# Optimization experiments

Measured on AMD Instinct MI355X. Metric: run time of the kernel, lower is better.

The kernel has to match this reference:

```python
import jax, jax.numpy as jnp
import numpy as np

B, S, D, H, DFF = 2, 2048, 1024, 16, 4096
DH = D // H
EPS = 1e-12


def _layer_norm(x, g, b):
    mu = jnp.mean(x, axis=-1, keepdims=True)
    var = jnp.mean(jnp.square(x - mu), axis=-1, keepdims=True)
    return (x - mu) * jax.lax.rsqrt(var + EPS) * g + b


def setup_inputs() -> dict:
    key = jax.random.key(0)
    ks = jax.random.split(key, 12)
    s = 0.02
    return {
        "query": jax.random.normal(ks[0], (B, S, D), jnp.float32),
        "key_in": jax.random.normal(ks[1], (B, S, D), jnp.float32),
        "value_in": jax.random.normal(ks[2], (B, S, D), jnp.float32),
        "attention_mask": jnp.zeros((B, 1, 1, S), jnp.float32),
        # weights stored [in, out] (i.e., torch Linear weight transposed)
        "Wq": jax.random.normal(ks[3], (D, D), jnp.float32) * s,
        "bq": jnp.zeros((D,), jnp.float32),
        "Wk": jax.random.normal(ks[4], (D, D), jnp.float32) * s,
        "bk": jnp.zeros((D,), jnp.float32),
        "Wv": jax.random.normal(ks[5], (D, D), jnp.float32) * s,
        "bv": jnp.zeros((D,), jnp.float32),
        "Wo": jax.random.normal(ks[6], (D, D), jnp.float32) * s,
        "bo": jnp.zeros((D,), jnp.float32),
        "ln1_g": jnp.ones((D,), jnp.float32),
        "ln1_b": jnp.zeros((D,), jnp.float32),
        "Wi": jax.random.normal(ks[7], (D, DFF), jnp.float32) * s,
        "bi": jnp.zeros((DFF,), jnp.float32),
        "Wd": jax.random.normal(ks[8], (DFF, D), jnp.float32) * s,
        "bd": jnp.zeros((D,), jnp.float32),
        "ln2_g": jnp.ones((D,), jnp.float32),
        "ln2_b": jnp.zeros((D,), jnp.float32),
    }


def reference(query, key_in, value_in, attention_mask, Wq, bq, Wk, bk, Wv, bv,
              Wo, bo, ln1_g, ln1_b, Wi, bi, Wd, bd, ln2_g, ln2_b):
    # projections -> [B, H, S, DH]
    q = (query @ Wq + bq).reshape(B, S, H, DH).transpose(0, 2, 1, 3)
    k = (key_in @ Wk + bk).reshape(B, S, H, DH).transpose(0, 2, 1, 3)
    v = (value_in @ Wv + bv).reshape(B, S, H, DH).transpose(0, 2, 1, 3)
    # eager attention: full [B,H,S,S] score matrix, as in the source
    scores = jnp.einsum("bhqd,bhkd->bhqk", q, k) / jnp.sqrt(jnp.float32(DH))
    scores = scores + attention_mask
    probs = jax.nn.softmax(scores, axis=-1)  # dropout p=0 -> identity
    ctx = jnp.einsum("bhqk,bhkd->bhqd", probs, v)
    ctx = ctx.transpose(0, 2, 1, 3).reshape(B, S, D)
    attn_out = ctx @ Wo + bo
    attn_out = _layer_norm(attn_out + query, ln1_g, ln1_b)
    inter = jax.nn.gelu(attn_out @ Wi + bi, approximate=False)
    layer_out = inter @ Wd + bd
    return _layer_norm(layer_out + attn_out, ln2_g, ln2_b)
```

## Files before the change

kernel.cpp:

```cpp
#include <hip/hip_runtime.h>
#include <hip/hip_bf16.h>
#include <cmath>

#define B_   2
#define S_   2048
#define D_   1024
#define H_   16
#define DFF_ 4096
#define DH_  64
#define M_   (B_*S_)

typedef __bf16 bfx8 __attribute__((ext_vector_type(8)));
typedef __bf16 bfx4 __attribute__((ext_vector_type(4)));
typedef float  fx4  __attribute__((ext_vector_type(4)));

__device__ __forceinline__ float fast_exp2(float x) {
  float r;
  asm volatile("v_exp_f32 %0, %1" : "=v"(r) : "v"(x));
  return r;
}

__device__ __forceinline__ float fast_erf(float x) {
  float ax = fabsf(x);
  float t  = __builtin_amdgcn_rcpf(fmaf(0.3275911f, ax, 1.0f));
  float p  = fmaf(1.061405429f, t, -1.453152027f);
  p = fmaf(p, t, 1.421413741f);
  p = fmaf(p, t, -0.284496736f);
  p = fmaf(p, t, 0.254829592f);
  p = p * t;
  float e  = fast_exp2(-ax * ax * 1.44269504f);
  float r  = 1.0f - p * e;
  return copysignf(r, x);
}

__device__ __forceinline__ void gload_lds16(const void* g, void* l) {
  __builtin_amdgcn_global_load_lds((__attribute__((address_space(1))) void*)(g),
                                   (__attribute__((address_space(3))) void*)(l),
                                   16, 0, 0);
}

struct PrepArgs {
  const float* win[6]; __bf16* wout[6];
  const float* cin[3]; __bf16* cout[3];
};

__global__ __launch_bounds__(256)
void prep_kernel(PrepArgs a) {
  int bid = blockIdx.x;
  if (bid < 12288) {
    __shared__ float t[32][33];
    int wsel, tr, tc, R, C;
    if (bid < 4096) {
      wsel = bid >> 10; int l = bid & 1023;
      tr = l >> 5; tc = l & 31; R = D_; C = D_;
    } else if (bid < 8192) {
      wsel = 4; int l = bid - 4096;
      tr = l >> 7; tc = l & 127; R = D_; C = DFF_;
    } else {
      wsel = 5; int l = bid - 8192;
      tr = l >> 5; tc = l & 31; R = DFF_; C = D_;
    }
    const float* in = a.win[wsel];
    __bf16* out = a.wout[wsel];
    int r0 = tr * 32, c0 = tc * 32;
    int tx = threadIdx.x & 31, ty = threadIdx.x >> 5;
#pragma unroll
    for (int j = 0; j < 4; ++j) {
      int r = ty + j * 8;
      t[r][tx] = in[(size_t)(r0 + r) * C + c0 + tx];
    }
    __syncthreads();
#pragma unroll
    for (int j = 0; j < 4; ++j) {
      int c = ty + j * 8;
      out[(size_t)(c0 + c) * R + r0 + tx] = (__bf16)t[tx][c];
    }
  } else {
    int l = bid - 12288;
    int z = l >> 12;
    int i = ((l & 4095) * 256 + threadIdx.x) * 4;
    float4 v = *(const float4*)(a.cin[z] + i);
    bfx4 o;
    o[0] = (__bf16)v.x; o[1] = (__bf16)v.y; o[2] = (__bf16)v.z; o[3] = (__bf16)v.w;
    *(bfx4*)(a.cout[z] + i) = o;
  }
}

template<int MODE, int TBN>
__global__ __launch_bounds__(256)
void gemm_kernel(const __bf16* __restrict__ A, const __bf16* __restrict__ Bt,
                 const float* __restrict__ bias, const void* __restrict__ res,
                 void* __restrict__ out, int Ndim, int Kdim) {
  __shared__ alignas(16) __bf16 As[2 * 128 * 64];
  __shared__ alignas(16) __bf16 Bs[2 * TBN * 64];
  const int tid  = threadIdx.x;
  const int lane = tid & 63;
  const int w    = tid >> 6;
  const int wm   = w >> 1, wn = w & 1;
  constexpr int NF = TBN / 32;

  const int gX  = gridDim.x;
  const int nwg = gridDim.x * gridDim.y;
  int lid = blockIdx.y * gX + blockIdx.x;
  int swz = (lid & 7) * (nwg >> 3) + (lid >> 3);
  const int m0 = (swz / gX) * 128, n0 = (swz % gX) * TBN;

  fx4 acc[4][NF];
#pragma unroll
  for (int i = 0; i < 4; ++i)
#pragma unroll
    for (int j = 0; j < NF; ++j) acc[i][j] = {0.f, 0.f, 0.f, 0.f};

  const int KT = Kdim / 64;

  auto stage = [&](int kt, int buf) {
    const int kb0 = kt * 64;
#pragma unroll
    for (int i = 0; i < 4; ++i) {
      int o   = tid * 16 + i * 4096;
      int row = o >> 7, cb = o & 127;
      int cbs = cb ^ ((row & 7) << 4);
      gload_lds16((const char*)A + ((size_t)(m0 + row) * Kdim + kb0) * 2 + cbs,
                  (char*)As + buf * 16384 + o);
    }
#pragma unroll
    for (int i = 0; i < NF; ++i) {
      int o   = tid * 16 + i * 4096;
      int row = o >> 7, cb = o & 127;
      int cbs = cb ^ ((row & 7) << 4);
      gload_lds16((const char*)Bt + ((size_t)(n0 + row) * Kdim + kb0) * 2 + cbs,
                  (char*)Bs + buf * (TBN * 128) + o);
    }
  };

  stage(0, 0);
  asm volatile("s_waitcnt vmcnt(0)" ::: "memory");
  __builtin_amdgcn_s_barrier();
  __builtin_amdgcn_sched_barrier(0);

  for (int kt = 0; kt < KT; ++kt) {
    if (kt + 1 < KT) stage(kt + 1, (kt + 1) & 1);
    __builtin_amdgcn_sched_barrier(0);
    if (kt > 0) {
      if (kt + 1 < KT) {
        if constexpr (TBN == 64) asm volatile("s_waitcnt vmcnt(6)" ::: "memory");
        else                     asm volatile("s_waitcnt vmcnt(8)" ::: "memory");
      } else {
        asm volatile("s_waitcnt vmcnt(0)" ::: "memory");
      }
      __builtin_amdgcn_s_barrier();
      __builtin_amdgcn_sched_barrier(0);
    }
    const char* Ab = (const char*)As + (kt & 1) * 16384;
    const char* Bb = (const char*)Bs + (kt & 1) * (TBN * 128);

#pragma unroll
    for (int kk = 0; kk < 2; ++kk) {
      bfx8 afr[4], bfr[NF];
      const int cb = kk * 64 + ((lane >> 4) << 4);
#pragma unroll
      for (int mf = 0; mf < 4; ++mf) {
        int row = wm * 64 + mf * 16 + (lane & 15);
        afr[mf] = *(const bfx8*)(Ab + row * 128 + (cb ^ ((row & 7) << 4)));
      }
#pragma unroll
      for (int nf = 0; nf < NF; ++nf) {
        int row = wn * (TBN / 2) + nf * 16 + (lane & 15);
        bfr[nf] = *(const bfx8*)(Bb + row * 128 + (cb ^ ((row & 7) << 4)));
      }
#pragma unroll
      for (int mf = 0; mf < 4; ++mf)
#pragma unroll
        for (int nf = 0; nf < NF; ++nf)
          acc[mf][nf] = __builtin_amdgcn_mfma_f32_16x16x32_bf16(afr[mf], bfr[nf],
                                                                acc[mf][nf], 0, 0, 0);
    }
    __builtin_amdgcn_s_barrier();
    __builtin_amdgcn_sched_barrier(0);
  }

#pragma unroll
  for (int mf = 0; mf < 4; ++mf) {
#pragma unroll
    for (int nf = 0; nf < NF; ++nf) {
      int col = n0 + wn * (TBN / 2) + nf * 16 + (lane & 15);
      float bvl = bias[col];
#pragma unroll
      for (int r = 0; r < 4; ++r) {
        int rowg = m0 + wm * 64 + mf * 16 + ((lane >> 4) << 2) + r;
        float v = acc[mf][nf][r] + bvl;
        if (MODE == 2) v = 0.5f * v * (1.0f + fast_erf(v * 0.70710678118654752f));
        if (MODE == 4) v += (float)((const __bf16*)res)[(size_t)rowg * Ndim + col];
        if (MODE == 1) ((float*)out)[(size_t)rowg * Ndim + col] = v;
        else           ((__bf16*)out)[(size_t)rowg * Ndim + col] = (__bf16)v;
      }
    }
  }
}

__device__ __forceinline__ void stage_a256(const __bf16* __restrict__ A, int m0,
                                           int Kdim, int tile, int h, char* Asm) {
  char* dst = Asm + (tile & 1) * 32768;
  const int kb0 = tile * 64;
  const int tid = threadIdx.x;
#pragma unroll
  for (int it = 0; it < 2; ++it) {
    int o = tid * 16 + it * 8192;
    int lrow = o >> 7, cb = o & 127;
    int r = (lrow & 63) + h * 64 + ((lrow >> 6) << 7);
    int csrc = cb ^ ((r & 7) << 4);
    gload_lds16((const char*)A + ((size_t)(m0 + r) * Kdim + kb0) * 2 + csrc,
                dst + r * 128 + cb);
  }
}
__device__ __forceinline__ void stage_b256(const __bf16* __restrict__ Bt, int n0,
                                           int Kdim, int tile, int h, char* Bsm) {
  char* dst = Bsm + (tile & 1) * 32768;
  const int kb0 = tile * 64;
  const int tid = threadIdx.x;
#pragma unroll
  for (int it = 0; it < 2; ++it) {
    int o = tid * 16 + it * 8192;
    int lrow = o >> 7, cb = o & 127;
    int r = h * 128 + lrow;
    int csrc = cb ^ ((r & 7) << 4);
    gload_lds16((const char*)Bt + ((size_t)(n0 + r) * Kdim + kb0) * 2 + csrc,
                dst + r * 128 + cb);
  }
}

template<int MODE>
__device__ __forceinline__ void gemm256_body(const __bf16* __restrict__ A,
                                             const __bf16* __restrict__ Bt,
                                             const float* __restrict__ bias,
                                             void* __restrict__ out,
                                             int Ndim, int Kdim, int m0, int n0) {
  extern __shared__ char smem[];
  char* Asm = smem;
  char* Bsm = smem + 65536;
  const int tid  = threadIdx.x;
  const int lane = tid & 63;
  const int w    = tid >> 6;
  const int wm   = w >> 2;
  const int wn   = w & 3;
  const int g    = lane >> 4;
  const int ql   = lane & 15;
  const int KT   = Kdim / 64;

  fx4 acc[8][4];
#pragma unroll
  for (int i = 0; i < 8; ++i)
#pragma unroll
    for (int j = 0; j < 4; ++j) acc[i][j] = {0.f, 0.f, 0.f, 0.f};

  stage_a256(A, m0, Kdim, 0, 0, Asm);
  stage_a256(A, m0, Kdim, 0, 1, Asm);
  stage_b256(Bt, n0, Kdim, 0, 0, Bsm);
  stage_b256(Bt, n0, Kdim, 0, 1, Bsm);
  stage_a256(A, m0, Kdim, 1, 0, Asm);
  asm volatile("s_waitcnt vmcnt(2)" ::: "memory");
  __builtin_amdgcn_s_barrier();
  __builtin_amdgcn_sched_barrier(0);

  for (int t = 0; t < KT; ++t) {
    const char* Ab = Asm + (t & 1) * 32768;
    const char* Bb = Bsm + (t & 1) * 32768;
#pragma unroll
    for (int p = 0; p < 4; ++p) {
      const int ah = p >> 1, kk = p & 1;
      if (p == 0 && t + 1 < KT) stage_a256(A, m0, Kdim, t + 1, 1, Asm);
      if (p == 1 && t + 1 < KT) stage_b256(Bt, n0, Kdim, t + 1, 0, Bsm);
      if (p == 2 && t + 1 < KT) stage_b256(Bt, n0, Kdim, t + 1, 1, Bsm);
      if (p == 3 && t + 2 < KT) stage_a256(A, m0, Kdim, t + 2, 0, Asm);
      __builtin_amdgcn_sched_barrier(0);

      bfx8 af[4], bf[4];
      const int cbv = kk * 64 + g * 16;
#pragma unroll
      for (int j = 0; j < 4; ++j) {
        int arow = wm * 128 + (ah * 4 + j) * 16 + ql;
        af[j] = *(const bfx8*)(Ab + arow * 128 + (cbv ^ ((arow & 7) << 4)));
      }
#pragma unroll
      for (int nf = 0; nf < 4; ++nf) {
        int brow = wn * 64 + nf * 16 + ql;
        bf[nf] = *(const bfx8*)(Bb + brow * 128 + (cbv ^ ((brow & 7) << 4)));
      }
      __builtin_amdgcn_sched_barrier(0);
      __builtin_amdgcn_s_barrier();
      asm volatile("s_waitcnt lgkmcnt(0)" ::: "memory");
      __builtin_amdgcn_sched_barrier(0);
      __builtin_amdgcn_s_setprio(1);
#pragma unroll
      for (int j = 0; j < 4; ++j)
#pragma unroll
        for (int nf = 0; nf < 4; ++nf)
          acc[ah * 4 + j][nf] = __builtin_amdgcn_mfma_f32_16x16x32_bf16(
              af[j], bf[nf], acc[ah * 4 + j][nf], 0, 0, 0);
      __builtin_amdgcn_s_setprio(0);
      __builtin_amdgcn_s_barrier();
      __builtin_amdgcn_sched_barrier(0);
    }
    if (t + 1 < KT) {
      if (t + 2 < KT) asm volatile("s_waitcnt vmcnt(2)" ::: "memory");
      else            asm volatile("s_waitcnt vmcnt(0)" ::: "memory");
      __builtin_amdgcn_s_barrier();
      __builtin_amdgcn_sched_barrier(0);
    }
  }

#pragma unroll
  for (int mf = 0; mf < 8; ++mf) {
#pragma unroll
    for (int nf = 0; nf < 4; ++nf) {
      int col = n0 + wn * 64 + nf * 16 + ql;
      float bvl = bias[col];
      if (MODE == 5) {
        int rowg0 = m0 + wm * 128 + mf * 16 + g * 4;
        int bb = rowg0 >> 11, s = rowg0 & 2047;
        int hh = col >> 6, dh = col & 63;
        bfx4 o;
#pragma unroll
        for (int r = 0; r < 4; ++r) o[r] = (__bf16)(acc[mf][nf][r] + bvl);
        *(bfx4*)((__bf16*)out + (((size_t)(bb * 16 + hh) * 64 + dh) * 2048 + s)) = o;
      } else {
#pragma unroll
        for (int r = 0; r < 4; ++r) {
          int rowg = m0 + wm * 128 + mf * 16 + g * 4 + r;
          float v = acc[mf][nf][r] + bvl;
          if (MODE == 2) v = 0.5f * v * (1.0f + fast_erf(v * 0.70710678118654752f));
          if (MODE == 1) ((float*)out)[(size_t)rowg * Ndim + col] = v;
          else          ((__bf16*)out)[(size_t)rowg * Ndim + col] = (__bf16)v;
        }
      }
    }
  }
}

template<int MODE>
__global__ __launch_bounds__(512)
void gemm256_kernel(const __bf16* __restrict__ A, const __bf16* __restrict__ Bt,
                    const float* __restrict__ bias, void* __restrict__ out,
                    int Ndim, int Kdim) {
  const int gX  = gridDim.x;
  const int nwg = gridDim.x * gridDim.y;
  int lid = blockIdx.y * gX + blockIdx.x;
  int swz = (lid & 7) * (nwg >> 3) + (lid >> 3);
  gemm256_body<MODE>(A, Bt, bias, out, Ndim, Kdim,
                     (swz / gX) * 256, (swz % gX) * 256);
}

struct QKVArgs {
  const __bf16* A[3]; const __bf16* Bt[3]; const float* bias[3]; __bf16* out[3];
};

__global__ __launch_bounds__(512)
void qkv256_kernel(QKVArgs args, int Ndim, int Kdim) {
  int z = blockIdx.z;
  const int gX  = gridDim.x;
  const int nwg = gridDim.x * gridDim.y;
  int lid = blockIdx.y * gX + blockIdx.x;
  int swz = (lid & 7) * (nwg >> 3) + (lid >> 3);
  int m0 = (swz / gX) * 256, n0 = (swz % gX) * 256;
  if (z == 2)
    gemm256_body<5>(args.A[2], args.Bt[2], args.bias[2], (void*)args.out[2],
                    Ndim, Kdim, m0, n0);
  else
    gemm256_body<0>(args.A[z], args.Bt[z], args.bias[z], (void*)args.out[z],
                    Ndim, Kdim, m0, n0);
}

__global__ __launch_bounds__(512)
void attn_kernel(const __bf16* __restrict__ Qb, const __bf16* __restrict__ Kb,
                 const __bf16* __restrict__ Vt, const float* __restrict__ mask,
                 __bf16* __restrict__ ctx) {
  __shared__ alignas(16) __bf16 Ks[3 * 64 * 64];
  __shared__ alignas(16) __bf16 Vs[3 * 64 * 64];
  __shared__ alignas(16) __bf16 Ps[8 * 16 * 64];
  __shared__ alignas(16) float  Ms[2048];

  const int tid  = threadIdx.x;
  const int lane = tid & 63;
  const int w    = tid >> 6;
  const int g    = lane >> 4;
  const int ql   = lane & 15;
  const int bh   = blockIdx.y;
  const int b    = bh >> 4;
  const int h    = bh & 15;
  const int q0   = blockIdx.x * 128;

  const size_t kbase  = ((size_t)(b * S_)) * D_ + h * DH_;
  const size_t vtbase = (size_t)bh * DH_ * S_;
  const int NT = S_ / 64;

  char* Qsm = (char*)Ps;
  const size_t qbase = ((size_t)(b * S_) + q0) * D_ + h * DH_;
#pragma unroll
  for (int i = 0; i < 2; ++i) {
    int o   = tid * 16 + i * 8192;
    int row = o >> 7, cb = o & 127;
    int cbs = cb ^ ((row & 7) << 4);
    gload_lds16((const char*)Qb + (qbase + (size_t)row * D_) * 2 + cbs, Qsm + o);
  }
  {
    int o = tid * 16;
    gload_lds16((const char*)mask + (size_t)b * S_ * 4 + o, (char*)Ms + o);
  }
  {
    int o   = tid * 16;
    int row = o >> 7, cb = o & 127;
    int cbs = cb ^ ((row & 7) << 4);
    gload_lds16((const char*)Kb + (kbase + (size_t)row * D_) * 2 + cbs, (char*)Ks + o);
    gload_lds16((const char*)Vt + (vtbase + (size_t)row * S_) * 2 + cbs, (char*)Vs + o);
    gload_lds16((const char*)Kb + (kbase + (size_t)(64 + row) * D_) * 2 + cbs,
                (char*)Ks + 8192 + o);
    gload_lds16((const char*)Vt + (vtbase + (size_t)row * S_ + 64) * 2 + cbs,
                (char*)Vs + 8192 + o);
  }
  asm volatile("s_waitcnt vmcnt(4)" ::: "memory");
  __builtin_amdgcn_s_barrier();
  __builtin_amdgcn_sched_barrier(0);

  {
    float4 mv = *(float4*)((char*)Ms + tid * 16);
    mv.x *= 1.44269504f; mv.y *= 1.44269504f;
    mv.z *= 1.44269504f; mv.w *= 1.44269504f;
    *(float4*)((char*)Ms + tid * 16) = mv;
  }

  bfx8 aq[2];
  {
    int row = w * 16 + ql;
#pragma unroll
    for (int kk = 0; kk < 2; ++kk) {
      int cb = kk * 64 + g * 16;
      aq[kk] = *(const bfx8*)(Qsm + row * 128 + (cb ^ ((row & 7) << 4)));
    }
  }
  __syncthreads();
  asm volatile("s_waitcnt vmcnt(2)" ::: "memory");
  __builtin_amdgcn_s_barrier();
  __builtin_amdgcn_sched_barrier(0);

  fx4 acc[4];
  fx4 accl = {0.f, 0.f, 0.f, 0.f};
#pragma unroll
  for (int d = 0; d < 4; ++d) acc[d] = {0.f, 0.f, 0.f, 0.f};

  bfx8 ones;
#pragma unroll
  for (int j = 0; j < 8; ++j) ones[j] = (__bf16)1.0f;

  char* pw = (char*)Ps + w * 2048;
  const float SCL = 0.18033688f;

  for (int t = 0; t < NT; ++t) {
    const int kv0 = t * 64;
    if (t + 2 < NT) {
      int o   = tid * 16;
      int row = o >> 7, cb = o & 127;
      int cbs = cb ^ ((row & 7) << 4);
      int nkv = kv0 + 128;
      int bo  = ((t + 2) % 3) * 8192;
      gload_lds16((const char*)Kb + (kbase + (size_t)(nkv + row) * D_) * 2 + cbs,
                  (char*)Ks + bo + o);
      gload_lds16((const char*)Vt + (vtbase + (size_t)row * S_ + nkv) * 2 + cbs,
                  (char*)Vs + bo + o);
    }
    __builtin_amdgcn_sched_barrier(0);
    const char* Kc = (const char*)Ks + (t % 3) * 8192;
    const char* Vc = (const char*)Vs + (t % 3) * 8192;

    fx4 sc[4];
#pragma unroll
    for (int nf = 0; nf < 4; ++nf) sc[nf] = {0.f, 0.f, 0.f, 0.f};
#pragma unroll
    for (int kk = 0; kk < 2; ++kk) {
      const int cb = kk * 64 + g * 16;
      bfx8 bk[4];
#pragma unroll
      for (int nf = 0; nf < 4; ++nf) {
        int row = nf * 16 + ql;
        bk[nf] = *(const bfx8*)(Kc + row * 128 + (cb ^ ((row & 7) << 4)));
      }
      __builtin_amdgcn_s_setprio(1);
#pragma unroll
      for (int nf = 0; nf < 4; ++nf)
        sc[nf] = __builtin_amdgcn_mfma_f32_16x16x32_bf16(bk[nf], aq[kk], sc[nf], 0, 0, 0);
      __builtin_amdgcn_s_setprio(0);
    }

    float sv[4][4];
#pragma unroll
    for (int nf = 0; nf < 4; ++nf) {
      float4 mk = *(const float4*)((const char*)Ms + (kv0 + nf * 16 + g * 4) * 4);
      sv[nf][0] = fast_exp2(fmaf(sc[nf][0], SCL, mk.x));
      sv[nf][1] = fast_exp2(fmaf(sc[nf][1], SCL, mk.y));
      sv[nf][2] = fast_exp2(fmaf(sc[nf][2], SCL, mk.z));
      sv[nf][3] = fast_exp2(fmaf(sc[nf][3], SCL, mk.w));
    }

#pragma unroll
    for (int nf = 0; nf < 4; ++nf) {
      bfx4 pv;
      pv[0] = (__bf16)sv[nf][0]; pv[1] = (__bf16)sv[nf][1];
      pv[2] = (__bf16)sv[nf][2]; pv[3] = (__bf16)sv[nf][3];
      int c = (nf * 32 + g * 8) ^ ((ql & 7) << 4);
      *(bfx4*)(pw + ql * 128 + c) = pv;
    }

    asm volatile("s_waitcnt lgkmcnt(0)" ::: "memory");
    __builtin_amdgcn_sched_barrier(0);

#pragma unroll
    for (int kk = 0; kk < 2; ++kk) {
      int prow = ql;
      int cb   = kk * 64 + g * 16;
      bfx8 ap  = *(const bfx8*)((const char*)pw + prow * 128 + (cb ^ ((prow & 7) << 4)));
      __builtin_amdgcn_s_setprio(1);
#pragma unroll
      for (int d = 0; d < 4; ++d) {
        int vrow = d * 16 + ql;
        bfx8 bv  = *(const bfx8*)(Vc + vrow * 128 + (cb ^ ((vrow & 7) << 4)));
        acc[d] = __builtin_amdgcn_mfma_f32_16x16x32_bf16(ap, bv, acc[d], 0, 0, 0);
      }
      accl = __builtin_amdgcn_mfma_f32_16x16x32_bf16(ap, ones, accl, 0, 0, 0);
      __builtin_amdgcn_s_setprio(0);
    }

    if (t + 1 < NT) {
      if (t + 2 < NT) asm volatile("s_waitcnt vmcnt(2)" ::: "memory");
      else            asm volatile("s_waitcnt vmcnt(0)" ::: "memory");
      __builtin_amdgcn_s_barrier();
      __builtin_amdgcn_sched_barrier(0);
    }
  }

#pragma unroll
  for (int r = 0; r < 4; ++r) {
    float inv = 1.0f / accl[r];
    int qrow = q0 + w * 16 + g * 4 + r;
    size_t base = ((size_t)(b * S_) + qrow) * D_ + h * DH_;
#pragma unroll
    for (int d = 0; d < 4; ++d)
      ctx[base + d * 16 + ql] = (__bf16)(acc[d][r] * inv);
  }
}

template<bool WRITE_BF16>
__global__ __launch_bounds__(256)
void ln_kernel(const __bf16* __restrict__ a,
               const float* __restrict__ g, const float* __restrict__ beta,
               float* __restrict__ outf, __bf16* __restrict__ outb) {
  const int row = blockIdx.x;
  const int tid = threadIdx.x;
  const size_t base = (size_t)row * D_;
  bfx4 xa = *(const bfx4*)(a + base + tid * 4);
  float x[4] = {(float)xa[0], (float)xa[1], (float)xa[2], (float)xa[3]};
  float s = x[0] + x[1] + x[2] + x[3];
#pragma unroll
  for (int m = 1; m < 64; m <<= 1) s += __shfl_xor(s, m);
  __shared__ float red[8];
  if ((tid & 63) == 0) red[tid >> 6] = s;
  __syncthreads();
  float mu = (red[0] + red[1] + red[2] + red[3]) * (1.0f / D_);
  float v0 = 0.f;
#pragma unroll
  for (int i = 0; i < 4; ++i) { float d = x[i] - mu; v0 += d * d; }
#pragma unroll
  for (int m = 1; m < 64; m <<= 1) v0 += __shfl_xor(v0, m);
  if ((tid & 63) == 0) red[4 + (tid >> 6)] = v0;
  __syncthreads();
  float var = (red[4] + red[5] + red[6] + red[7]) * (1.0f / D_);
  float rs = rsqrtf(var + 1e-12f);
#pragma unroll
  for (int i = 0; i < 4; ++i) {
    int col = tid * 4 + i;
    x[i] = (x[i] - mu) * rs * g[col] + beta[col];
  }
  if (WRITE_BF16) {
    bfx4 o;
    o[0] = (__bf16)x[0]; o[1] = (__bf16)x[1]; o[2] = (__bf16)x[2]; o[3] = (__bf16)x[3];
    *(bfx4*)(outb + base + tid * 4) = o;
  } else {
    *(float4*)(outf + base + tid * 4) = make_float4(x[0], x[1], x[2], x[3]);
  }
}

extern "C" void kernel_launch(void* const* d_in, const int* in_sizes, int n_in,
                              void* d_out, int out_size, void* d_ws, size_t ws_size,
                              hipStream_t stream) {
  const float* query    = (const float*)d_in[0];
  const float* key_in   = (const float*)d_in[1];
  const float* value_in = (const float*)d_in[2];
  const float* mask     = (const float*)d_in[3];
  const float* Wq = (const float*)d_in[4];  const float* bq = (const float*)d_in[5];
  const float* Wk = (const float*)d_in[6];  const float* bk = (const float*)d_in[7];
  const float* Wv = (const float*)d_in[8];  const float* bv = (const float*)d_in[9];
  const float* Wo = (const float*)d_in[10]; const float* bo = (const float*)d_in[11];
  const float* ln1g = (const float*)d_in[12]; const float* ln1b = (const float*)d_in[13];
  const float* Wi = (const float*)d_in[14]; const float* bi = (const float*)d_in[15];
  const float* Wd = (const float*)d_in[16]; const float* bd = (const float*)d_in[17];
  const float* ln2g = (const float*)d_in[18]; const float* ln2b = (const float*)d_in[19];

  char* ws = (char*)d_ws;
  const size_t MB = 1ull << 20;
  if (ws_size < 112 * MB) return;

  __bf16* xq   = (__bf16*)(ws + 0 * MB);
  __bf16* xk   = (__bf16*)(ws + 8 * MB);
  __bf16* xv   = (__bf16*)(ws + 16 * MB);
  __bf16* x1b  = (__bf16*)(ws + 16 * MB);
  __bf16* qb   = (__bf16*)(ws + 24 * MB);
  __bf16* inter= (__bf16*)(ws + 24 * MB);
  __bf16* kb   = (__bf16*)(ws + 32 * MB);
  __bf16* alinb= (__bf16*)(ws + 40 * MB);
  __bf16* vt   = (__bf16*)(ws + 48 * MB);
  __bf16* ctxb = (__bf16*)(ws + 56 * MB);
  __bf16* ffb  = (__bf16*)(ws + 56 * MB);
  __bf16* wqt  = (__bf16*)(ws + 88 * MB);
  __bf16* wkt  = (__bf16*)(ws + 90 * MB);
  __bf16* wvt  = (__bf16*)(ws + 92 * MB);
  __bf16* wot  = (__bf16*)(ws + 94 * MB);
  __bf16* wit  = (__bf16*)(ws + 96 * MB);
  __bf16* wdt  = (__bf16*)(ws + 104 * MB);

  dim3 b256(256);

  PrepArgs pa;
  pa.win[0] = Wq; pa.win[1] = Wk; pa.win[2] = Wv; pa.win[3] = Wo;
  pa.win[4] = Wi; pa.win[5] = Wd;
  pa.wout[0] = wqt; pa.wout[1] = wkt; pa.wout[2] = wvt; pa.wout[3] = wot;
  pa.wout[4] = wit; pa.wout[5] = wdt;
  pa.cin[0] = query; pa.cin[1] = key_in; pa.cin[2] = value_in;
  pa.cout[0] = xq;   pa.cout[1] = xk;    pa.cout[2] = xv;
  prep_kernel<<<dim3(24576), b256, 0, stream>>>(pa);

  QKVArgs qa;
  qa.A[0] = xq;  qa.A[1] = xk;  qa.A[2] = xv;
  qa.Bt[0] = wqt; qa.Bt[1] = wkt; qa.Bt[2] = wvt;
  qa.bias[0] = bq; qa.bias[1] = bk; qa.bias[2] = bv;
  qa.out[0] = qb; qa.out[1] = kb; qa.out[2] = vt;
  qkv256_kernel<<<dim3(D_ / 256, M_ / 256, 3), dim3(512), 131072, stream>>>(qa, D_, D_);

  attn_kernel<<<dim3(S_ / 128, B_ * H_), dim3(512), 0, stream>>>(qb, kb, vt, mask, ctxb);

  gemm_kernel<4, 64><<<dim3(D_ / 64, M_ / 128), b256, 0, stream>>>(ctxb, wot, bo, xq, (void*)alinb, D_, D_);

  ln_kernel<true><<<dim3(M_), b256, 0, stream>>>(alinb, ln1g, ln1b, nullptr, x1b);

  gemm256_kernel<2><<<dim3(DFF_ / 256, M_ / 256), dim3(512), 131072, stream>>>(x1b, wit, bi, (void*)inter, DFF_, D_);

  gemm_kernel<4, 64><<<dim3(D_ / 64, M_ / 128), b256, 0, stream>>>(inter, wdt, bd, x1b, (void*)ffb, D_, DFF_);

  ln_kernel<false><<<dim3(M_), b256, 0, stream>>>(ffb, ln2g, ln2b, (float*)d_out, nullptr);
}
```

Measured before the change: 240.7 us.

## Prescale mask in prep kernel and double-buffer K/V in attention

Moves the log2(e) scaling of the attention mask into the prep kernel, writing a scaled copy to the workspace. The attention kernel now reads mask values straight from global memory each iteration instead of staging them in LDS. K/V staging drops from triple to double buffering with a full vmcnt(0) wait each step. This cuts LDS use (possibly raising occupancy) but shortens the prefetch distance and puts a global load in the inner loop.

```diff
diff --git a/kernel.cpp b/kernel.cpp
--- a/kernel.cpp
+++ b/kernel.cpp
@@ -42,6 +42,7 @@
 struct PrepArgs {
   const float* win[6]; __bf16* wout[6];
   const float* cin[3]; __bf16* cout[3];
+  const float* min;    float* mout;
 };
 
 __global__ __launch_bounds__(256)
@@ -75,7 +76,7 @@
       int c = ty + j * 8;
       out[(size_t)(c0 + c) * R + r0 + tx] = (__bf16)t[tx][c];
     }
-  } else {
+  } else if (bid < 24576) {
     int l = bid - 12288;
     int z = l >> 12;
     int i = ((l & 4095) * 256 + threadIdx.x) * 4;
@@ -83,6 +84,12 @@
     bfx4 o;
     o[0] = (__bf16)v.x; o[1] = (__bf16)v.y; o[2] = (__bf16)v.z; o[3] = (__bf16)v.w;
     *(bfx4*)(a.cout[z] + i) = o;
+  } else {
+    int i = ((bid - 24576) * 256 + threadIdx.x) * 4;
+    float4 v = *(const float4*)(a.min + i);
+    v.x *= 1.44269504f; v.y *= 1.44269504f;
+    v.z *= 1.44269504f; v.w *= 1.44269504f;
+    *(float4*)(a.mout + i) = v;
   }
 }
 
@@ -372,13 +379,11 @@
 
 __global__ __launch_bounds__(512)
 void attn_kernel(const __bf16* __restrict__ Qb, const __bf16* __restrict__ Kb,
-                 const __bf16* __restrict__ Vt, const float* __restrict__ mask,
+                 const __bf16* __restrict__ Vt, const float* __restrict__ mask2,
                  __bf16* __restrict__ ctx) {
-  __shared__ alignas(16) __bf16 Ks[3 * 64 * 64];
-  __shared__ alignas(16) __bf16 Vs[3 * 64 * 64];
+  __shared__ alignas(16) __bf16 Ks[2 * 64 * 64];
+  __shared__ alignas(16) __bf16 Vs[2 * 64 * 64];
   __shared__ alignas(16) __bf16 Ps[8 * 16 * 64];
-  __shared__ alignas(16) float  Ms[2048];
-
   const int tid  = threadIdx.x;
   const int lane = tid & 63;
   const int w    = tid >> 6;
@@ -403,30 +408,15 @@
     gload_lds16((const char*)Qb + (qbase + (size_t)row * D_) * 2 + cbs, Qsm + o);
   }
   {
-    int o = tid * 16;
-    gload_lds16((const char*)mask + (size_t)b * S_ * 4 + o, (char*)Ms + o);
-  }
-  {
     int o   = tid * 16;
     int row = o >> 7, cb = o & 127;
     int cbs = cb ^ ((row & 7) << 4);
     gload_lds16((const char*)Kb + (kbase + (size_t)row * D_) * 2 + cbs, (char*)Ks + o);
     gload_lds16((const char*)Vt + (vtbase + (size_t)row * S_) * 2 + cbs, (char*)Vs + o);
-    gload_lds16((const char*)Kb + (kbase + (size_t)(64 + row) * D_) * 2 + cbs,
-                (char*)Ks + 8192 + o);
-    gload_lds16((const char*)Vt + (vtbase + (size_t)row * S_ + 64) * 2 + cbs,
-                (char*)Vs + 8192 + o);
-  }
-  asm volatile("s_waitcnt vmcnt(4)" ::: "memory");
+  }
+  asm volatile("s_waitcnt vmcnt(2)" ::: "memory");
   __builtin_amdgcn_s_barrier();
   __builtin_amdgcn_sched_barrier(0);
-
-  {
-    float4 mv = *(float4*)((char*)Ms + tid * 16);
-    mv.x *= 1.44269504f; mv.y *= 1.44269504f;
-    mv.z *= 1.44269504f; mv.w *= 1.44269504f;
-    *(float4*)((char*)Ms + tid * 16) = mv;
-  }
 
   bfx8 aq[2];
   {
@@ -438,7 +428,7 @@
     }
   }
   __syncthreads();
-  asm volatile("s_waitcnt vmcnt(2)" ::: "memory");
+  asm volatile("s_waitcnt vmcnt(0)" ::: "memory");
   __builtin_amdgcn_s_barrier();
   __builtin_amdgcn_sched_barrier(0);
 
@@ -453,23 +443,29 @@
 
   char* pw = (char*)Ps + w * 2048;
   const float SCL = 0.18033688f;
+  const float* mrow = mask2 + (size_t)b * S_;
 
   for (int t = 0; t < NT; ++t) {
     const int kv0 = t * 64;
-    if (t + 2 < NT) {
+    float4 mk[4];
+#pragma unroll
+    for (int nf = 0; nf < 4; ++nf)
+      mk[nf] = *(const float4*)(mrow + kv0 + nf * 16 + g * 4);
+    __builtin_amdgcn_sched_barrier(0);
+    if (t + 1 < NT) {
       int o   = tid * 16;
       int row = o >> 7, cb = o & 127;
       int cbs = cb ^ ((row & 7) << 4);
-      int nkv = kv0 + 128;
-      int bo  = ((t + 2) % 3) * 8192;
+      int nkv = kv0 + 64;
+      int bo  = ((t + 1) & 1) * 8192;
       gload_lds16((const char*)Kb + (kbase + (size_t)(nkv + row) * D_) * 2 + cbs,
                   (char*)Ks + bo + o);
       gload_lds16((const char*)Vt + (vtbase + (size_t)row * S_ + nkv) * 2 + cbs,
                   (char*)Vs + bo + o);
     }
     __builtin_amdgcn_sched_barrier(0);
-    const char* Kc = (const char*)Ks + (t % 3) * 8192;
-    const char* Vc = (const char*)Vs + (t % 3) * 8192;
+    const char* Kc = (const char*)Ks + (t & 1) * 8192;
+    const char* Vc = (const char*)Vs + (t & 1) * 8192;
 
     fx4 sc[4];
 #pragma unroll
@@ -493,11 +489,10 @@
     float sv[4][4];
 #pragma unroll
     for (int nf = 0; nf < 4; ++nf) {
-      float4 mk = *(const float4*)((const char*)Ms + (kv0 + nf * 16 + g * 4) * 4);
-      sv[nf][0] = fast_exp2(fmaf(sc[nf][0], SCL, mk.x));
-      sv[nf][1] = fast_exp2(fmaf(sc[nf][1], SCL, mk.y));
-      sv[nf][2] = fast_exp2(fmaf(sc[nf][2], SCL, mk.z));
-      sv[nf][3] = fast_exp2(fmaf(sc[nf][3], SCL, mk.w));
+      sv[nf][0] = fast_exp2(fmaf(sc[nf][0], SCL, mk[nf].x));
+      sv[nf][1] = fast_exp2(fmaf(sc[nf][1], SCL, mk[nf].y));
+      sv[nf][2] = fast_exp2(fmaf(sc[nf][2], SCL, mk[nf].z));
+      sv[nf][3] = fast_exp2(fmaf(sc[nf][3], SCL, mk[nf].w));
     }
 
 #pragma unroll
@@ -529,8 +524,7 @@
     }
 
     if (t + 1 < NT) {
-      if (t + 2 < NT) asm volatile("s_waitcnt vmcnt(2)" ::: "memory");
-      else            asm volatile("s_waitcnt vmcnt(0)" ::: "memory");
+      asm volatile("s_waitcnt vmcnt(0)" ::: "memory");
       __builtin_amdgcn_s_barrier();
       __builtin_amdgcn_sched_barrier(0);
     }
@@ -618,6 +612,7 @@
   __bf16* vt   = (__bf16*)(ws + 48 * MB);
   __bf16* ctxb = (__bf16*)(ws + 56 * MB);
   __bf16* ffb  = (__bf16*)(ws + 56 * MB);
+  float*  mask2= (float*)(ws + 72 * MB);
   __bf16* wqt  = (__bf16*)(ws + 88 * MB);
   __bf16* wkt  = (__bf16*)(ws + 90 * MB);
   __bf16* wvt  = (__bf16*)(ws + 92 * MB);
@@ -634,7 +629,8 @@
   pa.wout[4] = wit; pa.wout[5] = wdt;
   pa.cin[0] = query; pa.cin[1] = key_in; pa.cin[2] = value_in;
   pa.cout[0] = xq;   pa.cout[1] = xk;    pa.cout[2] = xv;
-  prep_kernel<<<dim3(24576), b256, 0, stream>>>(pa);
+  pa.min = mask; pa.mout = mask2;
+  prep_kernel<<<dim3(24580), b256, 0, stream>>>(pa);
 
   QKVArgs qa;
   qa.A[0] = xq;  qa.A[1] = xk;  qa.A[2] = xv;
@@ -643,7 +639,7 @@
   qa.out[0] = qb; qa.out[1] = kb; qa.out[2] = vt;
   qkv256_kernel<<<dim3(D_ / 256, M_ / 256, 3), dim3(512), 131072, stream>>>(qa, D_, D_);
 
-  attn_kernel<<<dim3(S_ / 128, B_ * H_), dim3(512), 0, stream>>>(qb, kb, vt, mask, ctxb);
+  attn_kernel<<<dim3(S_ / 128, B_ * H_), dim3(512), 0, stream>>>(qb, kb, vt, mask2, ctxb);
 
   gemm_kernel<4, 64><<<dim3(D_ / 64, M_ / 128), b256, 0, stream>>>(ctxb, wot, bo, xq, (void*)alinb, D_, D_);
 
```

Measured after the change: 238.5 us. Within noise of the previous version (-0.9%).
